# Optimization experiments

Measured on AMD Instinct MI355X. Metric: run time of the kernel, lower is better.

Reference implementation:

```python
import jax, jax.numpy as jnp
import numpy as np

B, S, D, H, E = 4, 2048, 2048, 4096, 8
TOP_K = 2
ENTROPY_WEIGHT = 0.1
MAX_USAGE_RATIO = 0.3


def setup_inputs() -> dict:
    key = jax.random.key(0)
    k0, k1, k2 = jax.random.split(key, 3)
    x = jax.random.normal(k0, (B, S, D), dtype=jnp.float32)
    gate_w = jax.random.normal(k1, (E, D), dtype=jnp.float32) * 0.02
    gate_b = jnp.zeros((E,), dtype=jnp.float32)
    expert_w = jax.random.normal(k2, (E, H, D), dtype=jnp.float32) * 0.02
    expert_b = jnp.zeros((E, H), dtype=jnp.float32)
    return {"x": x, "gate_w": gate_w, "gate_b": gate_b,
            "expert_w": expert_w, "expert_b": expert_b}


def reference(x, gate_w, gate_b, expert_w, expert_b):
    b, s, d = x.shape
    e, h, _ = expert_w.shape
    n = b * s
    xf = x.reshape(n, d)

    # gating
    gate_logits = xf @ gate_w.T + gate_b              # (N, E)
    gate_probs = jax.nn.softmax(gate_logits, axis=-1)
    entropy = (-jnp.sum(gate_probs * jnp.log(gate_probs + 1e-10), axis=-1)).mean()
    entropy_loss = ENTROPY_WEIGHT * entropy

    # top-k dispatch weights
    topk_probs, topk_idx = jax.lax.top_k(gate_probs, TOP_K)   # (N, K)
    combine = jnp.sum(jax.nn.one_hot(topk_idx, e, dtype=xf.dtype)
                      * topk_probs[..., None], axis=1)        # (N, E)

    # per-expert linear + weighted combine (loop over small fixed E)
    out = jnp.zeros((n, h), dtype=xf.dtype)
    for ei in range(e):
        out = out + combine[:, ei:ei + 1] * (xf @ expert_w[ei].T + expert_b[ei])

    # usage penalty (this batch's routing counts)
    counts = jnp.sum(jax.nn.one_hot(topk_idx, e, dtype=jnp.float32), axis=(0, 1))
    usage_ratios = counts / n
    overuse_penalty = jnp.sum(jax.nn.relu(usage_ratios - MAX_USAGE_RATIO))

    return out.reshape(b, s, h), entropy_loss + overuse_penalty
```

## Files before the change

kernel.cpp:

```cpp
#include <hip/hip_runtime.h>

constexpr int N_TOK = 8192;
constexpr int D_IN  = 2048;
constexpr int H_OUT = 4096;
constexpr int NEXP  = 8;
constexpr float ENT_W = 0.1f;
constexpr float MAX_USAGE = 0.3f;

constexpr int TM = 128;
constexpr int TH = 128;
constexpr int BK = 32;
constexpr int NKT = D_IN / BK;
constexpr int TILES_H = H_OUT / TH;
constexpr int TM_MAX  = N_TOK / TM;
constexpr int REGION  = 8192;
constexpr int BUFSZ   = TM * BK;

typedef __attribute__((ext_vector_type(8))) short bf16x8;
typedef __attribute__((ext_vector_type(4))) float f32x4;

__device__ __forceinline__ short f2bf(float f) {
    unsigned u = __float_as_uint(f);
    u += 0x7FFF + ((u >> 16) & 1);
    return (short)(u >> 16);
}

__device__ __forceinline__ void gload16(const void* g, void* l) {
    __builtin_amdgcn_global_load_lds(
        (const __attribute__((address_space(1))) unsigned int*)g,
        (__attribute__((address_space(3))) unsigned int*)l, 16, 0, 0);
}

__global__ __launch_bounds__(256) void gate_cvt_kernel(
    const float* __restrict__ x, const float* __restrict__ gate_w,
    const float* __restrict__ gate_b, int* __restrict__ topk_idx,
    float* __restrict__ topk_w, float* __restrict__ ent_partial,
    short* __restrict__ xb,
    const float* __restrict__ expert_w, short* __restrict__ wb)
{
    __shared__ float ent_s[4];
    const int wv = threadIdx.x >> 6;
    const int lane = threadIdx.x & 63;
    const int t = blockIdx.x * 4 + wv;

    float acc[NEXP];
#pragma unroll
    for (int e = 0; e < NEXP; ++e) acc[e] = 0.f;

    const float4* xr = (const float4*)(x + (size_t)t * D_IN);
    short* xbr = xb + (size_t)t * D_IN;
#pragma unroll
    for (int i = 0; i < D_IN / 256; ++i) {
        float4 xv = xr[lane + i * 64];
        short4 s4;
        s4.x = f2bf(xv.x); s4.y = f2bf(xv.y); s4.z = f2bf(xv.z); s4.w = f2bf(xv.w);
        *(short4*)(xbr + i * 256 + lane * 4) = s4;
#pragma unroll
        for (int e = 0; e < NEXP; ++e) {
            float4 gv = ((const float4*)(gate_w + e * D_IN))[lane + i * 64];
            acc[e] += xv.x * gv.x + xv.y * gv.y + xv.z * gv.z + xv.w * gv.w;
        }
    }
#pragma unroll
    for (int e = 0; e < NEXP; ++e)
#pragma unroll
        for (int m = 32; m >= 1; m >>= 1) acc[e] += __shfl_xor(acc[e], m, 64);

    if (lane == 0) {
        float lg[NEXP], p[NEXP];
        float mx = -1e30f;
#pragma unroll
        for (int e = 0; e < NEXP; ++e) { lg[e] = acc[e] + gate_b[e]; mx = fmaxf(mx, lg[e]); }
        float s = 0.f;
#pragma unroll
        for (int e = 0; e < NEXP; ++e) { p[e] = expf(lg[e] - mx); s += p[e]; }
        float inv = 1.f / s;
        float ent = 0.f;
#pragma unroll
        for (int e = 0; e < NEXP; ++e) { p[e] *= inv; ent -= p[e] * logf(p[e] + 1e-10f); }
        int e1 = 0; float b1 = p[0];
#pragma unroll
        for (int e = 1; e < NEXP; ++e) if (p[e] > b1) { b1 = p[e]; e1 = e; }
        int e2 = (e1 == 0) ? 1 : 0; float b2 = p[e2];
#pragma unroll
        for (int e = 0; e < NEXP; ++e)
            if (e != e1 && e != ((e1 == 0) ? 1 : 0) && p[e] > b2) { b2 = p[e]; e2 = e; }
        topk_idx[2 * t]     = e1;  topk_idx[2 * t + 1] = e2;
        topk_w[2 * t]       = b1;  topk_w[2 * t + 1]   = b2;
        ent_s[wv] = ent;
    }
    __syncthreads();
    if (threadIdx.x == 0)
        ent_partial[blockIdx.x] = ent_s[0] + ent_s[1] + ent_s[2] + ent_s[3];

    const int n8 = (NEXP * H_OUT * D_IN) / 8;
    int stride = gridDim.x * 256;
    for (int i = blockIdx.x * 256 + threadIdx.x; i < n8; i += stride) {
        const float4* p = (const float4*)expert_w + (size_t)i * 2;
        float4 a = p[0], b = p[1];
        bf16x8 v;
        v[0] = f2bf(a.x); v[1] = f2bf(a.y); v[2] = f2bf(a.z); v[3] = f2bf(a.w);
        v[4] = f2bf(b.x); v[5] = f2bf(b.y); v[6] = f2bf(b.z); v[7] = f2bf(b.w);
        *(bf16x8*)(wb + (size_t)i * 8) = v;
    }
}

__global__ __launch_bounds__(256) void scatter_kernel(
    const int* __restrict__ topk_idx, const float* __restrict__ topk_w,
    int* __restrict__ cursors, int* __restrict__ tok_list,
    float* __restrict__ w_list)
{
    __shared__ int lcnt[NEXP], lbase[NEXP];
    const int tid = threadIdx.x;
    const int t = blockIdx.x * 256 + tid;
    if (tid < NEXP) lcnt[tid] = 0;
    __syncthreads();
    int e0 = topk_idx[2 * t], e1 = topk_idx[2 * t + 1];
    float w0 = topk_w[2 * t], w1 = topk_w[2 * t + 1];
    int p0 = atomicAdd(&lcnt[e0], 1);
    int p1 = atomicAdd(&lcnt[e1], 1);
    __syncthreads();
    if (tid < NEXP) lbase[tid] = atomicAdd(&cursors[tid], lcnt[tid]);
    __syncthreads();
    int d0 = e0 * REGION + lbase[e0] + p0;
    int d1 = e1 * REGION + lbase[e1] + p1;
    tok_list[d0] = t;  w_list[d0] = w0;
    tok_list[d1] = t;  w_list[d1] = w1;
}

__global__ __launch_bounds__(256) void finalize_kernel(
    const int* __restrict__ counts, const float* __restrict__ ent_partial,
    float* __restrict__ loss_out)
{
    __shared__ float red[256];
    float s = 0.f;
    for (int i = threadIdx.x; i < N_TOK / 4; i += 256) s += ent_partial[i];
    red[threadIdx.x] = s;
    __syncthreads();
    for (int st = 128; st > 0; st >>= 1) {
        if (threadIdx.x < st) red[threadIdx.x] += red[threadIdx.x + st];
        __syncthreads();
    }
    if (threadIdx.x == 0) {
        float loss = ENT_W * red[0] / (float)N_TOK;
        for (int e = 0; e < NEXP; ++e) {
            float r = (float)counts[e] / (float)N_TOK - MAX_USAGE;
            if (r > 0.f) loss += r;
        }
        loss_out[0] = loss;
    }
}

__global__ __launch_bounds__(256, 4) void moe_gemm(
    const short* __restrict__ xb, const short* __restrict__ wb,
    const float* __restrict__ expert_b, const int* __restrict__ tok_list,
    const float* __restrict__ w_list, const int* __restrict__ counts,
    float* __restrict__ out)
{
    const int bid = blockIdx.x;
    const int e   = bid / (TM_MAX * TILES_H);
    const int rem = bid % (TM_MAX * TILES_H);
    const int tm  = rem / TILES_H;
    const int th  = rem % TILES_H;

    const int cnt = counts[e];
    if (tm * TM >= cnt) return;
    const int valid = cnt - tm * TM;
    const int hbase = th * TH;

    __shared__ __align__(16) short A_s[2][BUFSZ];
    __shared__ __align__(16) short B_s[2][BUFSZ];
    __shared__ int   tok_s[TM];
    __shared__ float wgt_s[TM];

    const int tid = threadIdx.x;
    if (tid < TM) {
        bool v = tid < valid;
        int src = e * REGION + tm * TM + tid;
        tok_s[tid] = v ? tok_list[src] : 0;
        wgt_s[tid] = v ? w_list[src] : 0.f;
    }
    __syncthreads();

    const int lane = tid & 63;
    const int wv = tid >> 6;

    const char* asrc[2];
    const char* bsrc[2];
    int dst_off[2];
#pragma unroll
    for (int j = 0; j < 2; ++j) {
        int c = wv * 2 + j;
        int r = c * 16 + (lane >> 2);
        int s2 = (lane & 3) ^ ((lane >> 3) & 3);
        asrc[j] = (const char*)(xb + (size_t)tok_s[r] * D_IN) + s2 * 16;
        bsrc[j] = (const char*)(wb + ((size_t)e * H_OUT + hbase + r) * D_IN) + s2 * 16;
        dst_off[j] = c * 512;
    }

    const int rr = lane & 15, kg = lane >> 4;
    const int wr = wv >> 1, wc = wv & 1;

    int aoff[4], boff[4];
#pragma unroll
    for (int mi = 0; mi < 4; ++mi) {
        int row = wr * 64 + mi * 16 + rr;
        aoff[mi] = row * 32 + (kg ^ ((row >> 1) & 3)) * 8;
        int rowb = wc * 64 + mi * 16 + rr;
        boff[mi] = rowb * 32 + (kg ^ ((rowb >> 1) & 3)) * 8;
    }

    f32x4 acc[4][4] = {};

#define STAGE_KT(buf)                                                      \
    {                                                                      \
        short* Aso = (short*)A_s[buf];                                     \
        short* Bso = (short*)B_s[buf];                                     \
        gload16(asrc[0], Aso + dst_off[0]); asrc[0] += BK * 2;             \
        gload16(bsrc[0], Bso + dst_off[0]); bsrc[0] += BK * 2;             \
        gload16(asrc[1], Aso + dst_off[1]); asrc[1] += BK * 2;             \
        gload16(bsrc[1], Bso + dst_off[1]); bsrc[1] += BK * 2;             \
    }

    STAGE_KT(0);
    STAGE_KT(1);
    asm volatile("s_waitcnt vmcnt(4)" ::: "memory");
    __builtin_amdgcn_sched_barrier(0);
    __builtin_amdgcn_s_barrier();

    for (int kt = 0; kt < NKT; ++kt) {
        const short* Ac = A_s[kt & 1];
        const short* Bc = B_s[kt & 1];

        bf16x8 af[4], bv[4];
#pragma unroll
        for (int mi = 0; mi < 4; ++mi) af[mi] = *(const bf16x8*)&Ac[aoff[mi]];
#pragma unroll
        for (int ni = 0; ni < 4; ++ni) bv[ni] = *(const bf16x8*)&Bc[boff[ni]];
        asm volatile("s_waitcnt lgkmcnt(0)" ::: "memory");
        __builtin_amdgcn_sched_barrier(0);
        __builtin_amdgcn_s_barrier();

        if (kt + 2 < NKT) STAGE_KT(kt & 1);

        __builtin_amdgcn_s_setprio(1);
#pragma unroll
        for (int mi = 0; mi < 4; ++mi)
#pragma unroll
            for (int ni = 0; ni < 4; ++ni)
                acc[mi][ni] = __builtin_amdgcn_mfma_f32_16x16x32_bf16(
                    af[mi], bv[ni], acc[mi][ni], 0, 0, 0);
        __builtin_amdgcn_s_setprio(0);

        if (kt + 2 < NKT) {
            asm volatile("s_waitcnt vmcnt(4)" ::: "memory");
        } else if (kt + 1 < NKT) {
            asm volatile("s_waitcnt vmcnt(0)" ::: "memory");
        }
        __builtin_amdgcn_sched_barrier(0);
        __builtin_amdgcn_s_barrier();
    }
#undef STAGE_KT

    const float* bias = expert_b + (size_t)e * H_OUT + hbase;
#pragma unroll
    for (int mi = 0; mi < 4; ++mi) {
#pragma unroll
        for (int ni = 0; ni < 4; ++ni) {
            int col = wc * 64 + ni * 16 + rr;
            float be = bias[col];
#pragma unroll
            for (int i = 0; i < 4; ++i) {
                int r = wr * 64 + mi * 16 + kg * 4 + i;
                if (r < valid) {
                    float val = wgt_s[r] * (acc[mi][ni][i] + be);
                    atomicAdd(&out[(size_t)tok_s[r] * H_OUT + hbase + col], val);
                }
            }
        }
    }
}

extern "C" void kernel_launch(void* const* d_in, const int* in_sizes, int n_in,
                              void* d_out, int out_size, void* d_ws, size_t ws_size,
                              hipStream_t stream) {
    const float* x        = (const float*)d_in[0];
    const float* gate_w   = (const float*)d_in[1];
    const float* gate_b   = (const float*)d_in[2];
    const float* expert_w = (const float*)d_in[3];
    const float* expert_b = (const float*)d_in[4];
    float* out = (float*)d_out;
    char* ws = (char*)d_ws;

    int*   topk_idx    = (int*)(ws);
    float* topk_w      = (float*)(ws + (64 << 10));
    int*   cursors     = (int*)(ws + (128 << 10));
    float* ent_partial = (float*)(ws + (128 << 10) + 256);
    int*   tok_list    = (int*)(ws + (160 << 10));
    float* w_list      = (float*)(ws + (416 << 10));
    short* xb          = (short*)(ws + (1ull << 20));
    short* wb          = (short*)(ws + (34ull << 20));

    hipMemsetAsync(cursors, 0, 64, stream);
    hipMemsetAsync(d_out, 0, (size_t)out_size * sizeof(float), stream);

    gate_cvt_kernel<<<N_TOK / 4, 256, 0, stream>>>(x, gate_w, gate_b, topk_idx,
                                                   topk_w, ent_partial, xb,
                                                   expert_w, wb);
    scatter_kernel<<<N_TOK / 256, 256, 0, stream>>>(topk_idx, topk_w, cursors,
                                                    tok_list, w_list);
    moe_gemm<<<NEXP * TM_MAX * TILES_H, 256, 0, stream>>>(
        xb, wb, expert_b, tok_list, w_list, cursors, out);
    finalize_kernel<<<1, 256, 0, stream>>>(cursors, ent_partial,
                                           out + (size_t)N_TOK * H_OUT);
}
```

Measured before the change: 652.2 us.

## Compact MoE tile schedule, pre-tile expert weights, and swizzle GEMM block order

A plan kernel builds a compact list of (expert, token-tile) descriptors, so the GEMM grid only covers real tiles instead of launching and early-exiting blocks for every possible tile. Expert weights are written in a tile-contiguous layout during bf16 conversion, so each K-step's B panel is one contiguous 8 KB chunk. Block IDs are swizzled across the grid to spread work and improve cache locality. Padding rows now repeat a valid token instead of token 0. The cost is an extra single-thread serial kernel launch and a strided read pattern during weight conversion.

```diff
diff --git a/kernel.cpp b/kernel.cpp
--- a/kernel.cpp
+++ b/kernel.cpp
@@ -12,9 +12,10 @@
 constexpr int BK = 32;
 constexpr int NKT = D_IN / BK;
 constexpr int TILES_H = H_OUT / TH;
-constexpr int TM_MAX  = N_TOK / TM;
 constexpr int REGION  = 8192;
 constexpr int BUFSZ   = TM * BK;
+constexpr int MAXTILES = N_TOK * 2 / TM + NEXP;
+constexpr int GRID_GEMM = MAXTILES * TILES_H;
 
 typedef __attribute__((ext_vector_type(8))) short bf16x8;
 typedef __attribute__((ext_vector_type(4))) float f32x4;
@@ -93,15 +94,22 @@
     if (threadIdx.x == 0)
         ent_partial[blockIdx.x] = ent_s[0] + ent_s[1] + ent_s[2] + ent_s[3];
 
-    const int n8 = (NEXP * H_OUT * D_IN) / 8;
+    const int total = NEXP << 20;
     int stride = gridDim.x * 256;
-    for (int i = blockIdx.x * 256 + threadIdx.x; i < n8; i += stride) {
-        const float4* p = (const float4*)expert_w + (size_t)i * 2;
-        float4 a = p[0], b = p[1];
+    for (int d = blockIdx.x * 256 + threadIdx.x; d < total; d += stride) {
+        int e    = d >> 20;
+        int th   = (d >> 15) & 31;
+        int kt   = (d >> 9) & 63;
+        int row  = (d >> 2) & 127;
+        int q    = d & 3;
+        int h = th * 128 + row;
+        int k = kt * 32 + q * 8;
+        const float4* s = (const float4*)(expert_w + ((size_t)e * H_OUT + h) * D_IN + k);
+        float4 a = s[0], b = s[1];
         bf16x8 v;
         v[0] = f2bf(a.x); v[1] = f2bf(a.y); v[2] = f2bf(a.z); v[3] = f2bf(a.w);
         v[4] = f2bf(b.x); v[5] = f2bf(b.y); v[6] = f2bf(b.z); v[7] = f2bf(b.w);
-        *(bf16x8*)(wb + (size_t)i * 8) = v;
+        *(bf16x8*)(wb + (size_t)d * 8) = v;
     }
 }
 
@@ -126,6 +134,27 @@
     int d1 = e1 * REGION + lbase[e1] + p1;
     tok_list[d0] = t;  w_list[d0] = w0;
     tok_list[d1] = t;  w_list[d1] = w1;
+}
+
+__global__ __launch_bounds__(64) void plan_kernel(
+    const int* __restrict__ counts, int* __restrict__ ntiles,
+    int* __restrict__ desc_e, int* __restrict__ desc_base,
+    int* __restrict__ desc_valid)
+{
+    if (threadIdx.x == 0) {
+        int n = 0;
+        for (int e = 0; e < NEXP; ++e) {
+            int cnt = counts[e];
+            for (int i = 0; i * TM < cnt; ++i) {
+                desc_e[n] = e;
+                desc_base[n] = e * REGION + i * TM;
+                int v = cnt - i * TM;
+                desc_valid[n] = v < TM ? v : TM;
+                ++n;
+            }
+        }
+        ntiles[0] = n;
+    }
 }
 
 __global__ __launch_bounds__(256) void finalize_kernel(
@@ -154,18 +183,19 @@
 __global__ __launch_bounds__(256, 4) void moe_gemm(
     const short* __restrict__ xb, const short* __restrict__ wb,
     const float* __restrict__ expert_b, const int* __restrict__ tok_list,
-    const float* __restrict__ w_list, const int* __restrict__ counts,
-    float* __restrict__ out)
+    const float* __restrict__ w_list, const int* __restrict__ ntiles,
+    const int* __restrict__ desc_e, const int* __restrict__ desc_base,
+    const int* __restrict__ desc_valid, float* __restrict__ out)
 {
     const int bid = blockIdx.x;
-    const int e   = bid / (TM_MAX * TILES_H);
-    const int rem = bid % (TM_MAX * TILES_H);
-    const int tm  = rem / TILES_H;
-    const int th  = rem % TILES_H;
-
-    const int cnt = counts[e];
-    if (tm * TM >= cnt) return;
-    const int valid = cnt - tm * TM;
+    const int swz = (bid & 7) * (GRID_GEMM / 8) + (bid >> 3);
+    const int tIdx = swz >> 5;
+    const int th   = swz & 31;
+    if (tIdx >= ntiles[0]) return;
+
+    const int e     = desc_e[tIdx];
+    const int base  = desc_base[tIdx];
+    const int valid = desc_valid[tIdx];
     const int hbase = th * TH;
 
     __shared__ __align__(16) short A_s[2][BUFSZ];
@@ -176,9 +206,8 @@
     const int tid = threadIdx.x;
     if (tid < TM) {
         bool v = tid < valid;
-        int src = e * REGION + tm * TM + tid;
-        tok_s[tid] = v ? tok_list[src] : 0;
-        wgt_s[tid] = v ? w_list[src] : 0.f;
+        tok_s[tid] = v ? tok_list[base + tid] : tok_list[base];
+        wgt_s[tid] = v ? w_list[base + tid] : 0.f;
     }
     __syncthreads();
 
@@ -188,13 +217,15 @@
     const char* asrc[2];
     const char* bsrc[2];
     int dst_off[2];
+    const char* bpanel = (const char*)wb +
+        ((size_t)(e * TILES_H + th)) * (64 * 8192);
 #pragma unroll
     for (int j = 0; j < 2; ++j) {
         int c = wv * 2 + j;
         int r = c * 16 + (lane >> 2);
         int s2 = (lane & 3) ^ ((lane >> 3) & 3);
         asrc[j] = (const char*)(xb + (size_t)tok_s[r] * D_IN) + s2 * 16;
-        bsrc[j] = (const char*)(wb + ((size_t)e * H_OUT + hbase + r) * D_IN) + s2 * 16;
+        bsrc[j] = bpanel + c * 1024 + (lane >> 2) * 64 + s2 * 16;
         dst_off[j] = c * 512;
     }
 
@@ -217,9 +248,9 @@
         short* Aso = (short*)A_s[buf];                                     \
         short* Bso = (short*)B_s[buf];                                     \
         gload16(asrc[0], Aso + dst_off[0]); asrc[0] += BK * 2;             \
-        gload16(bsrc[0], Bso + dst_off[0]); bsrc[0] += BK * 2;             \
+        gload16(bsrc[0], Bso + dst_off[0]); bsrc[0] += 8192;               \
         gload16(asrc[1], Aso + dst_off[1]); asrc[1] += BK * 2;             \
-        gload16(bsrc[1], Bso + dst_off[1]); bsrc[1] += BK * 2;             \
+        gload16(bsrc[1], Bso + dst_off[1]); bsrc[1] += 8192;               \
     }
 
     STAGE_KT(0);
@@ -295,7 +326,11 @@
     int*   topk_idx    = (int*)(ws);
     float* topk_w      = (float*)(ws + (64 << 10));
     int*   cursors     = (int*)(ws + (128 << 10));
-    float* ent_partial = (float*)(ws + (128 << 10) + 256);
+    int*   ntiles      = (int*)(ws + (128 << 10) + 64);
+    int*   desc_e      = (int*)(ws + (128 << 10) + 128);
+    int*   desc_base   = (int*)(ws + (128 << 10) + 1024);
+    int*   desc_valid  = (int*)(ws + (128 << 10) + 2048);
+    float* ent_partial = (float*)(ws + (132 << 10));
     int*   tok_list    = (int*)(ws + (160 << 10));
     float* w_list      = (float*)(ws + (416 << 10));
     short* xb          = (short*)(ws + (1ull << 20));
@@ -309,8 +344,11 @@
                                                    expert_w, wb);
     scatter_kernel<<<N_TOK / 256, 256, 0, stream>>>(topk_idx, topk_w, cursors,
                                                     tok_list, w_list);
-    moe_gemm<<<NEXP * TM_MAX * TILES_H, 256, 0, stream>>>(
-        xb, wb, expert_b, tok_list, w_list, cursors, out);
+    plan_kernel<<<1, 64, 0, stream>>>(cursors, ntiles, desc_e, desc_base,
+                                      desc_valid);
+    moe_gemm<<<GRID_GEMM, 256, 0, stream>>>(
+        xb, wb, expert_b, tok_list, w_list, ntiles, desc_e, desc_base,
+        desc_valid, out);
     finalize_kernel<<<1, 256, 0, stream>>>(cursors, ent_partial,
                                            out + (size_t)N_TOK * H_OUT);
 }
```

New measurement: 653.7 us. About the same (+0.2%).
